# Optimization experiments

Hardware: AMD Instinct MI355X
Metric: run time of the kernel (lower is better)

The kernel has to match this reference:

```python
import jax, jax.numpy as jnp
import numpy as np
from jax import lax

VOCAB, EMB, HID = 32000, 512, 1024
B, T = 16, 256

def setup_inputs() -> dict:
    key = jax.random.key(0)
    ks = jax.random.split(key, 8)
    s_emb = 1.0 / np.sqrt(EMB)
    s_hid = 1.0 / np.sqrt(HID)
    return {
        "x": jax.random.randint(ks[0], (B, T), 0, VOCAB),
        "emb_table": jax.random.normal(ks[1], (VOCAB, EMB), jnp.float32),
        "W_ih": jax.random.normal(ks[2], (4 * HID, EMB), jnp.float32) * s_hid,
        "W_hh": jax.random.normal(ks[3], (4 * HID, HID), jnp.float32) * s_hid,
        "b_ih": jax.random.normal(ks[4], (4 * HID,), jnp.float32) * s_hid,
        "b_hh": jax.random.normal(ks[5], (4 * HID,), jnp.float32) * s_hid,
        "head_W": jax.random.normal(ks[6], (VOCAB, HID), jnp.float32) * s_hid,
        "head_b": jax.random.normal(ks[7], (VOCAB,), jnp.float32) * s_hid,
    }

def reference(x, emb_table, W_ih, W_hh, b_ih, b_hh, head_W, head_b):
    # Embedding lookup: [B,T,E]
    e = emb_table[x]
    # Precompute input contributions to all 4 gates for all timesteps: [B,T,4H]
    xg = jnp.einsum("bte,ge->btg", e, W_ih) + b_ih
    H = W_hh.shape[1]
    h0 = jnp.zeros((x.shape[0], H), xg.dtype)
    c0 = jnp.zeros((x.shape[0], H), xg.dtype)

    def step(carry, xg_t):
        h, c = carry
        g = xg_t + h @ W_hh.T + b_hh  # [B,4H]
        i, f, gg, o = jnp.split(g, 4, axis=-1)  # PyTorch gate order: i,f,g,o
        i = jax.nn.sigmoid(i)
        f = jax.nn.sigmoid(f)
        gg = jnp.tanh(gg)
        o = jax.nn.sigmoid(o)
        c = f * c + i * gg
        h = o * jnp.tanh(c)
        return (h, c), h

    _, hs = lax.scan(step, (h0, c0), jnp.swapaxes(xg, 0, 1))  # hs: [T,B,H]
    h = jnp.swapaxes(hs, 0, 1)  # [B,T,H]
    logits = h @ head_W.T + head_b  # [B,T,V]
    return logits
```

## Files before the change

kernel.cpp:

```cpp
#include <hip/hip_runtime.h>
#include <hip/hip_bf16.h>
#include <cstdint>
#include <cstddef>

typedef __attribute__((ext_vector_type(8))) short short8;
typedef __attribute__((ext_vector_type(4))) float f32x4;
typedef __attribute__((ext_vector_type(4))) float f4;
typedef __attribute__((ext_vector_type(4))) short s4;
typedef __attribute__((ext_vector_type(4))) unsigned u32x4;
typedef unsigned short u16;
typedef unsigned long long u64;

#define VOCAB 32000
#define EMB   512
#define HID   1024
#define GDIM  4096
#define BATCH 16
#define SEQ   256
#define MTOT  4096
#define NBLK  64

#define SLAB  4096
#define BUFB  (NBLK * SLAB)

static __device__ __forceinline__ u16 f2bf(float f) {
  unsigned u = __builtin_bit_cast(unsigned, f);
  u += 0x7fffu + ((u >> 16) & 1u);
  return (u16)(u >> 16);
}

static __device__ __forceinline__ float fsig(float x) {
  return __builtin_amdgcn_rcpf(1.f + __expf(-x));
}
static __device__ __forceinline__ float ftanh(float x) {
  return 1.f - 2.f * __builtin_amdgcn_rcpf(1.f + __expf(2.f * x));
}

__global__ void cvt_bf16_v4(const float* __restrict__ in, u16* __restrict__ out, long n4) {
  long i = (long)blockIdx.x * blockDim.x + threadIdx.x;
  long stride = (long)gridDim.x * blockDim.x;
  for (; i < n4; i += stride) {
    f4 v = reinterpret_cast<const f4*>(in)[i];
    s4 o;
#pragma unroll
    for (int j = 0; j < 4; ++j) o[j] = (short)f2bf(v[j]);
    reinterpret_cast<s4*>(out)[i] = o;
  }
}

__global__ void embed_gather(const int* __restrict__ x, const float* __restrict__ emb,
                             u16* __restrict__ A) {
  int m = blockIdx.x;
  long base = (long)x[m] * EMB;
  int e4 = threadIdx.x;
  f4 v = reinterpret_cast<const f4*>(emb + base)[e4];
  s4 o;
#pragma unroll
  for (int j = 0; j < 4; ++j) o[j] = (short)f2bf(v[j]);
  reinterpret_cast<s4*>(A + (long)m * EMB)[e4] = o;
}

static __device__ __forceinline__ void gload_lds16(const void* g, void* l) {
  __builtin_amdgcn_global_load_lds(
      (const __attribute__((address_space(1))) void*)g,
      (__attribute__((address_space(3))) void*)l, 16, 0, 0);
}

template<int TXG>
__global__ __launch_bounds__(256) void gemm_bt(
    const u16* __restrict__ A, const u16* __restrict__ B,
    const float* __restrict__ bias, float* __restrict__ C,
    int M, int N, int K)
{
  __shared__ u16 As[128 * 32];
  __shared__ u16 Bs[128 * 32];
  int tid  = threadIdx.x;
  int lane = tid & 63;
  int wid  = tid >> 6;
  int m0 = blockIdx.y * 128, n0 = blockIdx.x * 128;
  int wm = (wid >> 1) * 64, wn = (wid & 1) * 64;
  f32x4 acc[4][4] = {};

  int c0 = wid * 128 + lane;
  int c1 = c0 + 64;
  const u16* ga0 = A + (long)(m0 + (c0 >> 2)) * K + (c0 & 3) * 8;
  const u16* ga1 = A + (long)(m0 + (c1 >> 2)) * K + (c1 & 3) * 8;
  const u16* gb0 = B + (long)(n0 + (c0 >> 2)) * K + (c0 & 3) * 8;
  const u16* gb1 = B + (long)(n0 + (c1 >> 2)) * K + (c1 & 3) * 8;
  u16* la0 = As + wid * 1024;
  u16* la1 = la0 + 512;
  u16* lb0 = Bs + wid * 1024;
  u16* lb1 = lb0 + 512;

  for (int kt = 0; kt < K; kt += 32) {
    __syncthreads();
    gload_lds16(ga0 + kt, la0);
    gload_lds16(ga1 + kt, la1);
    gload_lds16(gb0 + kt, lb0);
    gload_lds16(gb1 + kt, lb1);
    __syncthreads();
    short8 af[4], bf[4];
#pragma unroll
    for (int i = 0; i < 4; ++i) {
      af[i] = *reinterpret_cast<const short8*>(&As[(wm + i * 16 + (lane & 15)) * 32 + ((lane >> 4) << 3)]);
      bf[i] = *reinterpret_cast<const short8*>(&Bs[(wn + i * 16 + (lane & 15)) * 32 + ((lane >> 4) << 3)]);
    }
#pragma unroll
    for (int i = 0; i < 4; ++i)
#pragma unroll
      for (int j = 0; j < 4; ++j)
        acc[i][j] = __builtin_amdgcn_mfma_f32_16x16x32_bf16(af[i], bf[j], acc[i][j], 0, 0, 0);
  }

#pragma unroll
  for (int i = 0; i < 4; ++i) {
    int m = m0 + wm + i * 16 + ((lane >> 4) << 2);
#pragma unroll
    for (int j = 0; j < 4; ++j) {
      int n = n0 + wn + j * 16 + (lane & 15);
      float bv = bias[n];
#pragma unroll
      for (int jj = 0; jj < 4; ++jj) {
        int mm = m + jj;
        long row;
        if constexpr (TXG) {
          row = (long)(mm & (SEQ - 1)) * BATCH + (mm >> 8);
        } else {
          row = mm;
        }
        C[row * N + n] = acc[i][j][jj] + bv;
      }
    }
  }
}

__global__ __launch_bounds__(256, 1) void lstm_persist(
    const float* __restrict__ xg, const u16* __restrict__ Whh,
    const float* __restrict__ b_hh, unsigned* __restrict__ h_buf,
    u16* __restrict__ h_all)
{
  __shared__ float part[4][4][16][17];

  int tid = threadIdx.x;
  int w = tid >> 6, lane = tid & 63;
  int bid = blockIdx.x;
  int col0 = bid * 16;

  int r  = lane & 15;
  int ko = (lane >> 4) << 3;

  short8 Wf[8][4];
#pragma unroll
  for (int kk8 = 0; kk8 < 8; ++kk8)
#pragma unroll
    for (int g = 0; g < 4; ++g)
      Wf[kk8][g] = *reinterpret_cast<const short8*>(
          Whh + (long)(g * HID + col0 + r) * HID + (w * 256 + kk8 * 32 + ko));

  unsigned soff[2][4];
#pragma unroll
  for (int ph = 0; ph < 2; ++ph)
#pragma unroll
    for (int kk = 0; kk < 4; ++kk) {
      int p = w * 16 + ph * 8 + kk * 2 + (ko >> 4);
      soff[ph][kk] = (unsigned)(p * SLAB + r * 64 + (ko & 8) * 4);
    }
  const char* hbase = reinterpret_cast<const char*>(h_buf);

  int eb = tid >> 4, ec = tid & 15;
  const float* xgp = xg + (long)eb * GDIM + col0 + ec;
  float bias4[4];
#pragma unroll
  for (int g = 0; g < 4; ++g) bias4[g] = b_hh[g * HID + col0 + ec];
  u16* hap = h_all + (long)eb * SEQ * HID + col0 + ec;
  float creg = 0.f;

  __hip_atomic_store(&h_buf[(bid * SLAB / 4) + tid], 1u << 16,
                     __ATOMIC_RELAXED, __HIP_MEMORY_SCOPE_AGENT);

  float xv[4];
#pragma unroll
  for (int g = 0; g < 4; ++g) xv[g] = xgp[g * HID];

  for (int t = 0; t < SEQ; ++t) {
    unsigned want = (unsigned)(t + 1);
    const char* hb = hbase + ((t & 1) ? BUFB : 0);

    f32x4 a0 = {}, a1 = {}, a2 = {}, a3 = {};
#pragma unroll
    for (int ph = 0; ph < 2; ++ph) {
      u32x4 q[4][2];
      for (;;) {
#pragma unroll
        for (int kk = 0; kk < 4; ++kk) {
          const void* a = hb + soff[ph][kk];
          const void* b = hb + soff[ph][kk] + 16;
          asm volatile("global_load_dwordx4 %0, %1, off sc1"
                       : "=v"(q[kk][0]) : "v"(a));
          asm volatile("global_load_dwordx4 %0, %1, off sc1"
                       : "=v"(q[kk][1]) : "v"(b));
        }
        asm volatile("s_waitcnt vmcnt(0)" ::: "memory");
        __builtin_amdgcn_sched_barrier(0);
        bool allok = true;
#pragma unroll
        for (int kk = 0; kk < 4; ++kk)
#pragma unroll
          for (int v = 0; v < 2; ++v)
#pragma unroll
            for (int j = 0; j < 4; ++j)
              allok = allok && ((q[kk][v][j] >> 16) >= want);
        if (__all(allok)) break;
        __builtin_amdgcn_s_sleep(1);
      }

#pragma unroll
      for (int kk = 0; kk < 4; ++kk) {
        u32x4 wv;
        wv[0] = (q[kk][0][0] & 0xffffu) | (q[kk][0][1] << 16);
        wv[1] = (q[kk][0][2] & 0xffffu) | (q[kk][0][3] << 16);
        wv[2] = (q[kk][1][0] & 0xffffu) | (q[kk][1][1] << 16);
        wv[3] = (q[kk][1][2] & 0xffffu) | (q[kk][1][3] << 16);
        short8 av = __builtin_bit_cast(short8, wv);
        a0 = __builtin_amdgcn_mfma_f32_16x16x32_bf16(av, Wf[ph * 4 + kk][0], a0, 0, 0, 0);
        a1 = __builtin_amdgcn_mfma_f32_16x16x32_bf16(av, Wf[ph * 4 + kk][1], a1, 0, 0, 0);
        a2 = __builtin_amdgcn_mfma_f32_16x16x32_bf16(av, Wf[ph * 4 + kk][2], a2, 0, 0, 0);
        a3 = __builtin_amdgcn_mfma_f32_16x16x32_bf16(av, Wf[ph * 4 + kk][3], a3, 0, 0, 0);
      }
    }

#pragma unroll
    for (int j = 0; j < 4; ++j) {
      int batch = ((lane >> 4) << 2) + j;
      part[w][0][batch][lane & 15] = a0[j];
      part[w][1][batch][lane & 15] = a1[j];
      part[w][2][batch][lane & 15] = a2[j];
      part[w][3][batch][lane & 15] = a3[j];
    }
    __syncthreads();
    float pre[4];
#pragma unroll
    for (int g = 0; g < 4; ++g)
      pre[g] = part[0][g][eb][ec] + part[1][g][eb][ec] +
               part[2][g][eb][ec] + part[3][g][eb][ec] + xv[g] + bias4[g];
    float i_ = fsig(pre[0]);
    float f_ = fsig(pre[1]);
    float g_ = ftanh(pre[2]);
    float o_ = fsig(pre[3]);
    float cn = f_ * creg + i_ * g_;
    creg = cn;
    u16 hbf = f2bf(o_ * ftanh(cn));

    if (t + 1 < SEQ) {
      unsigned word = (unsigned)hbf | ((unsigned)(t + 2) << 16);
      __hip_atomic_store(
          &h_buf[(((t + 1) & 1) ? BUFB / 4 : 0) + (bid * SLAB / 4) + tid],
          word, __ATOMIC_RELAXED, __HIP_MEMORY_SCOPE_AGENT);
    }

    hap[(long)t * HID] = hbf;
    int tn = (t + 1 < SEQ) ? t + 1 : t;
#pragma unroll
    for (int g = 0; g < 4; ++g)
      xv[g] = xgp[(long)tn * BATCH * GDIM + g * HID];

    __syncthreads();
  }
}

extern "C" void kernel_launch(void* const* d_in, const int* in_sizes, int n_in,
                              void* d_out, int out_size, void* d_ws, size_t ws_size,
                              hipStream_t stream) {
  const int*   x      = (const int*)d_in[0];
  const float* emb    = (const float*)d_in[1];
  const float* W_ih   = (const float*)d_in[2];
  const float* W_hh   = (const float*)d_in[3];
  const float* b_ih   = (const float*)d_in[4];
  const float* b_hh   = (const float*)d_in[5];
  const float* head_W = (const float*)d_in[6];
  const float* head_b = (const float*)d_in[7];
  float* out = (float*)d_out;

  char* ws = (char*)d_ws;
  size_t off = 0;
  auto alloc = [&](size_t bytes) -> void* {
    void* p = ws + off;
    off += (bytes + 255) & ~(size_t)255;
    return p;
  };
  u16*      Aemb  = (u16*)alloc((size_t)MTOT * EMB * 2);
  u16*      Wih_b = (u16*)alloc((size_t)GDIM * EMB * 2);
  u16*      Whh_b = (u16*)alloc((size_t)GDIM * HID * 2);
  u16*      HW_b  = (u16*)alloc((size_t)VOCAB * HID * 2);
  float*    xg    = (float*)alloc((size_t)MTOT * GDIM * 4);
  u16*      h_all = (u16*)alloc((size_t)MTOT * HID * 2);
  unsigned* h_buf = (unsigned*)alloc((size_t)2 * BUFB);

  hipMemsetAsync(h_buf, 0, (size_t)2 * BUFB, stream);

  cvt_bf16_v4<<<1024, 256, 0, stream>>>(W_ih, Wih_b, (long)GDIM * EMB / 4);
  cvt_bf16_v4<<<1024, 256, 0, stream>>>(W_hh, Whh_b, (long)GDIM * HID / 4);
  cvt_bf16_v4<<<2048, 256, 0, stream>>>(head_W, HW_b, (long)VOCAB * HID / 4);
  embed_gather<<<MTOT, 128, 0, stream>>>(x, emb, Aemb);

  gemm_bt<1><<<dim3(GDIM / 128, MTOT / 128), 256, 0, stream>>>(
      Aemb, Wih_b, b_ih, xg, MTOT, GDIM, EMB);

  {
    const float* xgc = xg;
    const u16* whc = Whh_b;
    void* args[] = {(void*)&xgc, (void*)&whc, (void*)&b_hh,
                    (void*)&h_buf, (void*)&h_all};
    hipLaunchCooperativeKernel((const void*)lstm_persist, dim3(NBLK), dim3(256),
                               args, 0, stream);
  }

  gemm_bt<0><<<dim3(VOCAB / 128, MTOT / 128), 256, 0, stream>>>(
      h_all, HW_b, head_b, out, MTOT, VOCAB, HID);
}
```

Before: 1.241 ms.

## Widen GEMM K-tile to 64 with XOR-swizzled LDS and block remapping

The bf16 GEMM now stages 64-wide K tiles instead of 32, which halves the number of barrier pairs per K loop. Global loads are XOR-swizzled so that LDS fragment reads avoid bank conflicts. Workgroup IDs are remapped across 8 groups to improve L2 locality, presumably per XCD. The cost is double the LDS per block and more address arithmetic.

```diff
diff --git a/kernel.cpp b/kernel.cpp
--- a/kernel.cpp
+++ b/kernel.cpp
@@ -72,52 +72,74 @@
     const float* __restrict__ bias, float* __restrict__ C,
     int M, int N, int K)
 {
-  __shared__ u16 As[128 * 32];
-  __shared__ u16 Bs[128 * 32];
+  __shared__ u16 As[128 * 64];
+  __shared__ u16 Bs[128 * 64];
   int tid  = threadIdx.x;
   int lane = tid & 63;
   int wid  = tid >> 6;
-  int m0 = blockIdx.y * 128, n0 = blockIdx.x * 128;
+
+  int nwg = gridDim.x * gridDim.y;
+  int id  = blockIdx.y * gridDim.x + blockIdx.x;
+  int id2 = (id & 7) * (nwg >> 3) + (id >> 3);
+  int bx  = id2 % gridDim.x, by = id2 / gridDim.x;
+  int m0 = by * 128, n0 = bx * 128;
+
   int wm = (wid >> 1) * 64, wn = (wid & 1) * 64;
+  int r  = lane & 15;
+  int hi = lane >> 4;
   f32x4 acc[4][4] = {};
 
-  int c0 = wid * 128 + lane;
-  int c1 = c0 + 64;
-  const u16* ga0 = A + (long)(m0 + (c0 >> 2)) * K + (c0 & 3) * 8;
-  const u16* ga1 = A + (long)(m0 + (c1 >> 2)) * K + (c1 & 3) * 8;
-  const u16* gb0 = B + (long)(n0 + (c0 >> 2)) * K + (c0 & 3) * 8;
-  const u16* gb1 = B + (long)(n0 + (c1 >> 2)) * K + (c1 & 3) * 8;
-  u16* la0 = As + wid * 1024;
-  u16* la1 = la0 + 512;
-  u16* lb0 = Bs + wid * 1024;
-  u16* lb1 = lb0 + 512;
-
-  for (int kt = 0; kt < K; kt += 32) {
+  const u16* gaj[4];
+  const u16* gbj[4];
+  u16* laj[4];
+  u16* lbj[4];
+#pragma unroll
+  for (int j = 0; j < 4; ++j) {
+    int c   = wid * 256 + j * 64 + lane;
+    int row = c >> 3;
+    int gl  = (c & 7) ^ (row & 7);
+    gaj[j] = A + (long)(m0 + row) * K + gl * 8;
+    gbj[j] = B + (long)(n0 + row) * K + gl * 8;
+    laj[j] = As + wid * 2048 + j * 512;
+    lbj[j] = Bs + wid * 2048 + j * 512;
+  }
+
+  for (int kt = 0; kt < K; kt += 64) {
     __syncthreads();
-    gload_lds16(ga0 + kt, la0);
-    gload_lds16(ga1 + kt, la1);
-    gload_lds16(gb0 + kt, lb0);
-    gload_lds16(gb1 + kt, lb1);
+#pragma unroll
+    for (int j = 0; j < 4; ++j) {
+      gload_lds16(gaj[j] + kt, laj[j]);
+      gload_lds16(gbj[j] + kt, lbj[j]);
+    }
     __syncthreads();
-    short8 af[4], bf[4];
-#pragma unroll
-    for (int i = 0; i < 4; ++i) {
-      af[i] = *reinterpret_cast<const short8*>(&As[(wm + i * 16 + (lane & 15)) * 32 + ((lane >> 4) << 3)]);
-      bf[i] = *reinterpret_cast<const short8*>(&Bs[(wn + i * 16 + (lane & 15)) * 32 + ((lane >> 4) << 3)]);
-    }
-#pragma unroll
-    for (int i = 0; i < 4; ++i)
-#pragma unroll
-      for (int j = 0; j < 4; ++j)
-        acc[i][j] = __builtin_amdgcn_mfma_f32_16x16x32_bf16(af[i], bf[j], acc[i][j], 0, 0, 0);
+    short8 af[2][4], bf[2][4];
+#pragma unroll
+    for (int ks = 0; ks < 2; ++ks)
+#pragma unroll
+      for (int i = 0; i < 4; ++i) {
+        int ra = wm + i * 16 + r;
+        int rb = wn + i * 16 + r;
+        af[ks][i] = *reinterpret_cast<const short8*>(
+            &As[ra * 64 + ((ks * 4 + hi) ^ (ra & 7)) * 8]);
+        bf[ks][i] = *reinterpret_cast<const short8*>(
+            &Bs[rb * 64 + ((ks * 4 + hi) ^ (rb & 7)) * 8]);
+      }
+#pragma unroll
+    for (int ks = 0; ks < 2; ++ks)
+#pragma unroll
+      for (int i = 0; i < 4; ++i)
+#pragma unroll
+        for (int j = 0; j < 4; ++j)
+          acc[i][j] = __builtin_amdgcn_mfma_f32_16x16x32_bf16(
+              af[ks][i], bf[ks][j], acc[i][j], 0, 0, 0);
   }
 
 #pragma unroll
   for (int i = 0; i < 4; ++i) {
-    int m = m0 + wm + i * 16 + ((lane >> 4) << 2);
+    int m = m0 + wm + i * 16 + (hi << 2);
 #pragma unroll
     for (int j = 0; j < 4; ++j) {
-      int n = n0 + wn + j * 16 + (lane & 15);
+      int n = n0 + wn + j * 16 + r;
       float bv = bias[n];
 #pragma unroll
       for (int jj = 0; jj < 4; ++jj) {
```

Measured after the change: 1.199 ms. -3.4%, faster.
